# Performance work log

Measured on AMD Instinct MI355X. Metric: run time of the kernel, lower is better.

The kernel has to match this reference:

```python
import jax, jax.numpy as jnp
import numpy as np
import math

B, LQ, LK, D, DV = 16, 2048, 2048, 256, 256


def setup_inputs() -> dict:
    key = jax.random.key(0)
    k1, k2, k3, k4 = jax.random.split(key, 4)
    query = jax.random.normal(k1, (B, LQ, D), dtype=jnp.float32)
    key_t = jax.random.normal(k2, (B, LK, D), dtype=jnp.float32)
    value = jax.random.normal(k3, (B, LK, DV), dtype=jnp.float32)
    valid_length = jax.random.randint(k4, (B,), 0, LK, dtype=jnp.int32)
    return {"query": query, "key": key_t, "value": value, "valid_length": valid_length}


def reference(query, key, value, valid_length):
    # scores: [B, Lq, Lk]
    d = query.shape[-1]
    scores = jnp.einsum("bqd,bkd->bqk", query, key) / math.sqrt(d)
    # SequenceMask in the torch code sets masked positions to 0 (NOT -inf)
    # BEFORE the softmax; reproduce that exact behavior.
    kpos = jnp.arange(scores.shape[-1])  # [Lk]
    mask = kpos[None, None, :] < valid_length[:, None, None]  # [B,1,Lk] -> broadcast over Lq
    scores = jnp.where(mask, scores, 0.0)
    attn = jax.nn.softmax(scores, axis=-1)
    # Dropout is identity in eval mode.
    return jnp.einsum("bqk,bkv->bqv", attn, value)
```

## Files before the change

### kernel.cpp

```cpp
#include <hip/hip_runtime.h>

#define LQg 2048
#define LKg 2048
#define DDg 256
#define NBg 16
#define KVB 32
#define NTILES 64
#define SMAX 2

typedef unsigned int uint;
typedef unsigned short ushort;
typedef unsigned char uchar;
typedef __attribute__((ext_vector_type(8))) __bf16 bf16x8;
typedef __attribute__((ext_vector_type(16))) float f32x16;

static __device__ __forceinline__ uint pack2(float a, float b) {
    ushort ua = __builtin_bit_cast(ushort, (__bf16)a);
    ushort ub = __builtin_bit_cast(ushort, (__bf16)b);
    return (uint)ua | ((uint)ub << 16);
}

static __device__ __forceinline__ f32x16 mfma32(bf16x8 a, bf16x8 b, f32x16 c) {
    return __builtin_amdgcn_mfma_f32_32x32x16_bf16(a, b, c, 0, 0, 0);
}

typedef const __attribute__((address_space(1))) uchar* gas_t;
typedef __attribute__((address_space(3))) uchar* las_t;
static __device__ __forceinline__ void gl_lds16(const void* g, void* l) {
    __builtin_amdgcn_global_load_lds((gas_t)g, (las_t)l, 16, 0, 0);
}

__global__ __launch_bounds__(256) void prep_k(const float* __restrict__ K,
                                              uchar* __restrict__ Kimg) {
    const uint gid = blockIdx.x * 256 + threadIdx.x;
    const uint d8 = gid & 31;
    const uint row = (gid >> 5) & 31;
    const uint t = (gid >> 10) & 63;
    const uint b = gid >> 16;
    const float* src = K + (((size_t)b * LKg + t * KVB + row) * DDg + d8 * 8);
    float4 a = *(const float4*)src;
    float4 c = *(const float4*)(src + 4);
    uint4 u;
    u.x = pack2(a.x, a.y); u.y = pack2(a.z, a.w);
    u.z = pack2(c.x, c.y); u.w = pack2(c.z, c.w);
    const size_t base = ((size_t)(b * NTILES + t)) << 14;
    const uint off = row * 512 + ((d8 * 16) ^ ((row & 7) << 4));
    *(uint4*)(Kimg + base + off) = u;
}

__global__ __launch_bounds__(256) void prep_v(const float* __restrict__ V,
                                              uchar* __restrict__ Vimg) {
    const uint gid = blockIdx.x * 256 + threadIdx.x;
    const uint dv = gid & 255;
    const uint t = (gid >> 8) & 63;
    const uint b = gid >> 14;
    const uint rot = 4 * ((dv >> 1) & 15);
    uchar* base = Vimg + (((size_t)(b * NTILES + t)) << 14) + dv * 64;
    const float* src = V + ((size_t)b * LKg + t * KVB) * DDg + dv;
#pragma unroll
    for (int kq = 0; kq < 8; ++kq) {
        float v0 = src[(kq * 4 + 0) * DDg];
        float v1 = src[(kq * 4 + 1) * DDg];
        float v2 = src[(kq * 4 + 2) * DDg];
        float v3 = src[(kq * 4 + 3) * DDg];
        const uint o = (8 * kq + rot) & 63;
        *(uint*)(base + o) = pack2(v0, v1);
        *(uint*)(base + ((o + 4) & 63)) = pack2(v2, v3);
    }
}

__global__ void tv_partial_k(const float* __restrict__ V, const int* __restrict__ vlen,
                             float* __restrict__ part) {
    const int c = blockIdx.x, b = blockIdx.y, t = threadIdx.x;
    const int vl = vlen[b];
    int bnd = ((vl + 31) >> 5) << 5;
    if (bnd > LKg) bnd = LKg;
    const int k0 = c * 128, k1 = k0 + 128;
    int lo = k0 > bnd ? k0 : bnd;
    float s = 0.f;
    for (int k = lo; k < k1; ++k) s += V[((size_t)(b * LKg + k)) * DDg + t];
    part[(size_t)(b * 16 + c) * DDg + t] = s;
}

__global__ void tv_reduce_k(const float* __restrict__ part, float* __restrict__ TV) {
    const int b = blockIdx.x, t = threadIdx.x;
    float s = 0.f;
    for (int c = 0; c < 16; ++c) s += part[(size_t)(b * 16 + c) * DDg + t];
    TV[b * DDg + t] = s;
}

template <int IMG>
__global__ __launch_bounds__(256, 1) void attn_k(
    const float* __restrict__ Qg, const float* __restrict__ Kg,
    const float* __restrict__ Vg, const uchar* __restrict__ Kimg,
    const uchar* __restrict__ Vimg, const int* __restrict__ vlen,
    const float* __restrict__ TV, float* __restrict__ Og,
    ushort* __restrict__ Pacc, float* __restrict__ Mp, float* __restrict__ Ep,
    int S, int use_tail) {
    __shared__ alignas(16) uchar sK[2][KVB * 512];
    __shared__ alignas(16) uchar sV[2][256 * 64];

    const int tid = threadIdx.x;
    const int lane = tid & 63;
    const int w = tid >> 6;
    const int lq = lane & 31;
    const int h = lane >> 5;
    const int qb = blockIdx.x & 15;
    const int b = blockIdx.x >> 4;
    const int s = blockIdx.y;
    const int q = qb * 128 + w * 32 + lq;
    const int vl = vlen[b];

    const float SCALE = 0.09016844136f;

    const int nt = use_tail ? ((vl + KVB - 1) / KVB) : NTILES;
    const int chunk = (nt + S - 1) / S;
    const int t0 = s * chunk;
    const int t1 = (t0 + chunk < nt) ? (t0 + chunk) : nt;

    if (S > 1 && t0 >= t1) {
        if (h == 0) {
            const size_t pidx = ((size_t)(s * NBg + b)) * LQg + q;
            Mp[pidx] = -1e30f;
            Ep[pidx] = 0.f;
        }
        return;
    }

    const int swzK = (lq & 7) << 4;
    const int rotv = (lq >> 1) * 4;

    int cur = 0;
    if (IMG) {
        const uchar* gK = Kimg + (((size_t)(b * NTILES + t0)) << 14) + tid * 16;
        const uchar* gV = Vimg + (((size_t)(b * NTILES + t0)) << 14) + tid * 16;
#pragma unroll
        for (int i = 0; i < 4; ++i) {
            gl_lds16(gK + i * 4096, &sK[0][i * 4096 + tid * 16]);
            gl_lds16(gV + i * 4096, &sV[0][i * 4096 + tid * 16]);
        }
    }

    bf16x8 qf[16];
    {
        const float* qp = Qg + ((size_t)(b * LQg + q)) * DDg + h * 8;
#pragma unroll
        for (int c = 0; c < 16; ++c) {
            float4 a = *(const float4*)(qp + c * 16);
            float4 bb = *(const float4*)(qp + c * 16 + 4);
            uint4 u;
            u.x = pack2(a.x * SCALE, a.y * SCALE);
            u.y = pack2(a.z * SCALE, a.w * SCALE);
            u.z = pack2(bb.x * SCALE, bb.y * SCALE);
            u.w = pack2(bb.z * SCALE, bb.w * SCALE);
            qf[c] = __builtin_bit_cast(bf16x8, u);
        }
    }

    if (!IMG) {
#pragma unroll
        for (int i = 0; i < 4; ++i) {
            const int cid = i * 256 + tid;
            const int d8 = cid & 31, row = cid >> 5;
            const float* src = Kg + (((size_t)b * LKg + t0 * KVB + row) * DDg + d8 * 8);
            float4 a = *(const float4*)src;
            float4 c = *(const float4*)(src + 4);
            uint4 u;
            u.x = pack2(a.x, a.y); u.y = pack2(a.z, a.w);
            u.z = pack2(c.x, c.y); u.w = pack2(c.z, c.w);
            *(uint4*)(&sK[0][row * 512 + ((d8 * 16) ^ ((row & 7) << 4))]) = u;
        }
        {
            const int dv = tid;
            const uint rot = 4 * ((dv >> 1) & 15);
            const float* src = Vg + ((size_t)b * LKg + t0 * KVB) * DDg + dv;
            uchar* dst = &sV[0][dv * 64];
#pragma unroll
            for (int kq = 0; kq < 8; ++kq) {
                float v0 = src[(kq * 4 + 0) * DDg];
                float v1 = src[(kq * 4 + 1) * DDg];
                float v2 = src[(kq * 4 + 2) * DDg];
                float v3 = src[(kq * 4 + 3) * DDg];
                const uint o = (8 * kq + rot) & 63;
                *(uint*)(dst + o) = pack2(v0, v1);
                *(uint*)(dst + ((o + 4) & 63)) = pack2(v2, v3);
            }
        }
    }

    f32x16 acc[8];
#pragma unroll
    for (int i = 0; i < 8; ++i)
#pragma unroll
        for (int j = 0; j < 16; ++j) acc[i][j] = 0.f;

    float m = -1e30f, ell = 0.f;

    __syncthreads();

    for (int t = t0; t < t1; ++t) {
        const int k0 = t * KVB;

        if (t + 1 < t1) {
            if (IMG) {
                const uchar* gK = Kimg + (((size_t)(b * NTILES + t + 1)) << 14) + tid * 16;
                const uchar* gV = Vimg + (((size_t)(b * NTILES + t + 1)) << 14) + tid * 16;
#pragma unroll
                for (int i = 0; i < 4; ++i) {
                    gl_lds16(gK + i * 4096, &sK[cur ^ 1][i * 4096 + tid * 16]);
                    gl_lds16(gV + i * 4096, &sV[cur ^ 1][i * 4096 + tid * 16]);
                }
            } else {
                const int k1 = (t + 1) * KVB;
#pragma unroll
                for (int i = 0; i < 4; ++i) {
                    const int cid = i * 256 + tid;
                    const int d8 = cid & 31, row = cid >> 5;
                    const float* src = Kg + (((size_t)b * LKg + k1 + row) * DDg + d8 * 8);
                    float4 a = *(const float4*)src;
                    float4 c = *(const float4*)(src + 4);
                    uint4 u;
                    u.x = pack2(a.x, a.y); u.y = pack2(a.z, a.w);
                    u.z = pack2(c.x, c.y); u.w = pack2(c.z, c.w);
                    *(uint4*)(&sK[cur ^ 1][row * 512 + ((d8 * 16) ^ ((row & 7) << 4))]) = u;
                }
                {
                    const int dv = tid;
                    const uint rot = 4 * ((dv >> 1) & 15);
                    const float* src = Vg + ((size_t)b * LKg + k1) * DDg + dv;
                    uchar* dst = &sV[cur ^ 1][dv * 64];
#pragma unroll
                    for (int kq = 0; kq < 8; ++kq) {
                        float v0 = src[(kq * 4 + 0) * DDg];
                        float v1 = src[(kq * 4 + 1) * DDg];
                        float v2 = src[(kq * 4 + 2) * DDg];
                        float v3 = src[(kq * 4 + 3) * DDg];
                        const uint o = (8 * kq + rot) & 63;
                        *(uint*)(dst + o) = pack2(v0, v1);
                        *(uint*)(dst + ((o + 4) & 63)) = pack2(v2, v3);
                    }
                }
            }
        }

        const uchar* sKc = sK[cur];
        const uchar* sVc = sV[cur];
        f32x16 s0;
#pragma unroll
        for (int j = 0; j < 16; ++j) s0[j] = 0.f;
#pragma unroll
        for (int c = 0; c < 16; ++c) {
            bf16x8 kf = *(const bf16x8*)(sKc + lq * 512 + ((c * 32 + h * 16) ^ swzK));
            s0 = mfma32(kf, qf[c], s0);
        }

        if (k0 + KVB > vl) {
            const int kb0 = k0 + 4 * h;
#pragma unroll
            for (int r = 0; r < 16; ++r) {
                const int key0 = kb0 + (r & 3) + 8 * (r >> 2);
                if (key0 >= vl) s0[r] = 0.f;
            }
        }

        float mt = s0[0];
#pragma unroll
        for (int r = 1; r < 16; ++r) mt = fmaxf(mt, s0[r]);
        mt = fmaxf(mt, __shfl_xor(mt, 32));
        if (mt > m + 8.f) {
            const float mn = fmaxf(m, mt);
            const float sf = exp2f(m - mn);
            ell *= sf;
#pragma unroll
            for (int i = 0; i < 8; ++i) acc[i] *= sf;
            m = mn;
        }
        float rs = 0.f;
#pragma unroll
        for (int r = 0; r < 16; ++r) { s0[r] = exp2f(s0[r] - m); rs += s0[r]; }
        rs += __shfl_xor(rs, 32);
        ell += rs;

        bf16x8 pf[2];
#pragma unroll
        for (int kc = 0; kc < 2; ++kc) {
            const int bb = kc * 8;
            uint w0 = pack2(s0[bb + 0], s0[bb + 1]);
            uint w1 = pack2(s0[bb + 2], s0[bb + 3]);
            uint w2 = pack2(s0[bb + 4], s0[bb + 5]);
            uint w3 = pack2(s0[bb + 6], s0[bb + 7]);
            uint e0 = __shfl_xor(w0, 32);
            uint e1 = __shfl_xor(w1, 32);
            uint e2 = __shfl_xor(w2, 32);
            uint e3 = __shfl_xor(w3, 32);
            uint4 u;
            u.x = h ? e2 : w0;
            u.y = h ? e3 : w1;
            u.z = h ? w2 : e0;
            u.w = h ? w3 : e1;
            pf[kc] = __builtin_bit_cast(bf16x8, u);
        }

#pragma unroll
        for (int kc = 0; kc < 2; ++kc) {
            const int kk = kc * 16 + h * 8;
            const uint o0 = (uint)((2 * kk + rotv) & 63);
            const uint o1 = (uint)((2 * kk + 4 + rotv) & 63);
            const uint o2 = (uint)((2 * kk + 8 + rotv) & 63);
            const uint o3 = (uint)((2 * kk + 12 + rotv) & 63);
#pragma unroll
            for (int dt = 0; dt < 8; ++dt) {
                const uchar* base = sVc + dt * 2048 + lq * 64;
                uint4 u;
                u.x = *(const uint*)(base + o0);
                u.y = *(const uint*)(base + o1);
                u.z = *(const uint*)(base + o2);
                u.w = *(const uint*)(base + o3);
                acc[dt] = mfma32(__builtin_bit_cast(bf16x8, u), pf[kc], acc[dt]);
            }
        }

        __syncthreads();
        cur ^= 1;
    }

    if (S > 1) {
        const size_t pidx = ((size_t)(s * NBg + b)) * LQg + q;
        if (h == 0) { Mp[pidx] = m; Ep[pidx] = ell; }
        ushort* pp = Pacc + pidx * DDg;
#pragma unroll
        for (int dt = 0; dt < 8; ++dt) {
#pragma unroll
            for (int rg = 0; rg < 4; ++rg) {
                const int dv0 = dt * 32 + 8 * rg + 4 * h;
                uint2 uu;
                uu.x = pack2(acc[dt][rg * 4 + 0], acc[dt][rg * 4 + 1]);
                uu.y = pack2(acc[dt][rg * 4 + 2], acc[dt][rg * 4 + 3]);
                *(uint2*)(pp + dv0) = uu;
            }
        }
        return;
    }

    if (use_tail) {
        const int bnd = nt * KVB;
        const int cnt = LKg - bnd;
        if (cnt > 0) {
            if (m < -8.f) {
                const float sf = exp2f(m);
                ell *= sf;
#pragma unroll
                for (int i = 0; i < 8; ++i) acc[i] *= sf;
                m = 0.f;
            }
            const float pt = exp2f(-m);
            ell += (float)cnt * pt;
            const float* tp = TV + b * DDg + h * 4;
#pragma unroll
            for (int dt = 0; dt < 8; ++dt) {
#pragma unroll
                for (int rg = 0; rg < 4; ++rg) {
                    float4 tv = *(const float4*)(tp + dt * 32 + rg * 8);
                    acc[dt][rg * 4 + 0] += pt * tv.x;
                    acc[dt][rg * 4 + 1] += pt * tv.y;
                    acc[dt][rg * 4 + 2] += pt * tv.z;
                    acc[dt][rg * 4 + 3] += pt * tv.w;
                }
            }
        }
    }
    const float inv = 1.f / ell;
    float* op = Og + ((size_t)(b * LQg + q)) * DDg + h * 4;
#pragma unroll
    for (int dt = 0; dt < 8; ++dt) {
#pragma unroll
        for (int rg = 0; rg < 4; ++rg) {
            float4 o;
            o.x = acc[dt][rg * 4 + 0] * inv;
            o.y = acc[dt][rg * 4 + 1] * inv;
            o.z = acc[dt][rg * 4 + 2] * inv;
            o.w = acc[dt][rg * 4 + 3] * inv;
            *(float4*)(op + dt * 32 + rg * 8) = o;
        }
    }
}

__global__ void combine_k(const ushort* __restrict__ Pacc, const float* __restrict__ Mp,
                          const float* __restrict__ Ep, const float* __restrict__ TV,
                          const int* __restrict__ vlen, float* __restrict__ Og, int S) {
    const int t = threadIdx.x;
    const int qi = t >> 6;
    const int dv4 = (t & 63) * 4;
    const long long bq0 = (long long)blockIdx.x * 4;
    const int b = (int)(bq0 >> 11);
    const int q = (int)(bq0 & 2047) + qi;
    const int vl = vlen[b];
    int bnd = ((vl + 31) >> 5) << 5;
    if (bnd > LKg) bnd = LKg;
    const int cnt = LKg - bnd;

    float mi[SMAX], ei[SMAX];
    float M = (cnt > 0) ? 0.f : -1e30f;
    for (int s = 0; s < S; ++s) {
        const size_t pidx = ((size_t)(s * NBg + b)) * LQg + q;
        mi[s] = Mp[pidx];
        ei[s] = Ep[pidx];
        if (ei[s] > 0.f) M = fmaxf(M, mi[s]);
    }
    float L = 0.f;
    float o0 = 0.f, o1 = 0.f, o2 = 0.f, o3 = 0.f;
    for (int s = 0; s < S; ++s) {
        if (ei[s] > 0.f) {
            const float wg = exp2f(mi[s] - M);
            L += ei[s] * wg;
            const size_t pidx = ((size_t)(s * NBg + b)) * LQg + q;
            uint2 uu = *(const uint2*)(Pacc + pidx * DDg + dv4);
            o0 += wg * __builtin_bit_cast(float, (uu.x & 0xFFFFu) << 16);
            o1 += wg * __builtin_bit_cast(float, (uu.x & 0xFFFF0000u));
            o2 += wg * __builtin_bit_cast(float, (uu.y & 0xFFFFu) << 16);
            o3 += wg * __builtin_bit_cast(float, (uu.y & 0xFFFF0000u));
        }
    }
    if (cnt > 0) {
        const float pt = exp2f(-M);
        L += (float)cnt * pt;
        float4 tv = *(const float4*)(TV + b * DDg + dv4);
        o0 += pt * tv.x; o1 += pt * tv.y; o2 += pt * tv.z; o3 += pt * tv.w;
    }
    const float inv = 1.f / L;
    float4 o; o.x = o0 * inv; o.y = o1 * inv; o.z = o2 * inv; o.w = o3 * inv;
    *(float4*)(Og + ((size_t)(b * LQg + q)) * DDg + dv4) = o;
}

extern "C" void kernel_launch(void* const* d_in, const int* in_sizes, int n_in,
                              void* d_out, int out_size, void* d_ws, size_t ws_size,
                              hipStream_t stream) {
    const float* Q = (const float*)d_in[0];
    const float* K = (const float*)d_in[1];
    const float* V = (const float*)d_in[2];
    const int* vlen = (const int*)d_in[3];
    float* out = (float*)d_out;

    const size_t off_part = 0;
    const size_t off_TV = 262144;
    const size_t off_K = 524288;
    const size_t imgsz = (size_t)NBg * NTILES * 16384;
    const size_t off_V = off_K + imgsz;
    const size_t off_M = off_V + imgsz;
    const size_t mpsz = (size_t)SMAX * NBg * LQg * 4;
    const size_t off_E = off_M + mpsz;
    const size_t off_P = off_E + mpsz;
    const size_t accsz = (size_t)NBg * LQg * DDg * 2;

    const size_t need_tail = off_TV + (size_t)NBg * DDg * 4;
    const size_t need_img = off_M;
    const size_t need_split = off_P + (size_t)SMAX * accsz;

    const int use_tail = (ws_size >= need_tail) ? 1 : 0;
    const int use_img = (ws_size >= need_img) ? 1 : 0;
    const int S = (use_img && use_tail && ws_size >= need_split) ? SMAX : 1;

    float* part = (float*)((char*)d_ws + off_part);
    float* TV = (float*)((char*)d_ws + off_TV);
    uchar* Kimg = (uchar*)d_ws + off_K;
    uchar* Vimg = (uchar*)d_ws + off_V;
    float* Mp = (float*)((char*)d_ws + off_M);
    float* Ep = (float*)((char*)d_ws + off_E);
    ushort* Pacc = (ushort*)((char*)d_ws + off_P);

    if (use_tail) {
        tv_partial_k<<<dim3(16, 16), 256, 0, stream>>>(V, vlen, part);
        tv_reduce_k<<<dim3(16), 256, 0, stream>>>(part, TV);
    }
    if (use_img) {
        prep_k<<<dim3(4096), 256, 0, stream>>>(K, Kimg);
        prep_v<<<dim3(1024), 256, 0, stream>>>(V, Vimg);
        attn_k<1><<<dim3(256, S), 256, 0, stream>>>(Q, K, V, Kimg, Vimg, vlen, TV, out,
                                                    Pacc, Mp, Ep, S, use_tail);
    } else {
        attn_k<0><<<dim3(256, 1), 256, 0, stream>>>(Q, K, V, Kimg, Vimg, vlen, TV, out,
                                                    Pacc, Mp, Ep, 1, use_tail);
    }
    if (S > 1) {
        combine_k<<<dim3(NBg * LQg / 4), 256, 0, stream>>>(Pacc, Mp, Ep, TV, vlen, out, S);
    }
}
```

Before: 217.1 us.

## Double KV tile to 64 keys, add phase-rotated tile order and MFMA priority

Result: faster. 207.7 us (-4.4%).

```diff
diff --git a/kernel.cpp b/kernel.cpp
--- a/kernel.cpp
+++ b/kernel.cpp
@@ -4,8 +4,9 @@
 #define LKg 2048
 #define DDg 256
 #define NBg 16
-#define KVB 32
-#define NTILES 64
+#define KVB 64
+#define NTILES 32
+#define TSHIFT 15
 #define SMAX 2
 
 typedef unsigned int uint;
@@ -24,6 +25,10 @@
     return __builtin_amdgcn_mfma_f32_32x32x16_bf16(a, b, c, 0, 0, 0);
 }
 
+static __device__ __forceinline__ int vrot(int dv) {
+    return (((dv & 15) * 8) + (((dv >> 2) & 7) * 16)) & 127;
+}
+
 typedef const __attribute__((address_space(1))) uchar* gas_t;
 typedef __attribute__((address_space(3))) uchar* las_t;
 static __device__ __forceinline__ void gl_lds16(const void* g, void* l) {
@@ -34,8 +39,8 @@
                                               uchar* __restrict__ Kimg) {
     const uint gid = blockIdx.x * 256 + threadIdx.x;
     const uint d8 = gid & 31;
-    const uint row = (gid >> 5) & 31;
-    const uint t = (gid >> 10) & 63;
+    const uint row = (gid >> 5) & 63;
+    const uint t = (gid >> 11) & 31;
     const uint b = gid >> 16;
     const float* src = K + (((size_t)b * LKg + t * KVB + row) * DDg + d8 * 8);
     float4 a = *(const float4*)src;
@@ -43,7 +48,7 @@
     uint4 u;
     u.x = pack2(a.x, a.y); u.y = pack2(a.z, a.w);
     u.z = pack2(c.x, c.y); u.w = pack2(c.z, c.w);
-    const size_t base = ((size_t)(b * NTILES + t)) << 14;
+    const size_t base = ((size_t)(b * NTILES + t)) << TSHIFT;
     const uint off = row * 512 + ((d8 * 16) ^ ((row & 7) << 4));
     *(uint4*)(Kimg + base + off) = u;
 }
@@ -52,20 +57,20 @@
                                               uchar* __restrict__ Vimg) {
     const uint gid = blockIdx.x * 256 + threadIdx.x;
     const uint dv = gid & 255;
-    const uint t = (gid >> 8) & 63;
-    const uint b = gid >> 14;
-    const uint rot = 4 * ((dv >> 1) & 15);
-    uchar* base = Vimg + (((size_t)(b * NTILES + t)) << 14) + dv * 64;
+    const uint t = (gid >> 8) & 31;
+    const uint b = gid >> 13;
+    const uint rot = (uint)vrot((int)dv);
+    uchar* base = Vimg + (((size_t)(b * NTILES + t)) << TSHIFT) + dv * 128;
     const float* src = V + ((size_t)b * LKg + t * KVB) * DDg + dv;
 #pragma unroll
-    for (int kq = 0; kq < 8; ++kq) {
+    for (int kq = 0; kq < 16; ++kq) {
         float v0 = src[(kq * 4 + 0) * DDg];
         float v1 = src[(kq * 4 + 1) * DDg];
         float v2 = src[(kq * 4 + 2) * DDg];
         float v3 = src[(kq * 4 + 3) * DDg];
-        const uint o = (8 * kq + rot) & 63;
-        *(uint*)(base + o) = pack2(v0, v1);
-        *(uint*)(base + ((o + 4) & 63)) = pack2(v2, v3);
+        const uint o = (8 * kq + rot) & 127;
+        uint2 uu; uu.x = pack2(v0, v1); uu.y = pack2(v2, v3);
+        *(uint2*)(base + o) = uu;
     }
 }
 
@@ -73,7 +78,7 @@
                              float* __restrict__ part) {
     const int c = blockIdx.x, b = blockIdx.y, t = threadIdx.x;
     const int vl = vlen[b];
-    int bnd = ((vl + 31) >> 5) << 5;
+    int bnd = ((vl + 63) >> 6) << 6;
     if (bnd > LKg) bnd = LKg;
     const int k0 = c * 128, k1 = k0 + 128;
     int lo = k0 > bnd ? k0 : bnd;
@@ -98,7 +103,7 @@
     ushort* __restrict__ Pacc, float* __restrict__ Mp, float* __restrict__ Ep,
     int S, int use_tail) {
     __shared__ alignas(16) uchar sK[2][KVB * 512];
-    __shared__ alignas(16) uchar sV[2][256 * 64];
+    __shared__ alignas(16) uchar sV[2][256 * 128];
 
     const int tid = threadIdx.x;
     const int lane = tid & 63;
@@ -128,14 +133,18 @@
     }
 
     const int swzK = (lq & 7) << 4;
-    const int rotv = (lq >> 1) * 4;
+    const int rotv = vrot(lq);
+
+    const int len = t1 - t0;
+    const int ph = ((blockIdx.x ^ s) & 1) ? (len >> 1) : 0;
+    const int ts0 = t0 + ph;
 
     int cur = 0;
     if (IMG) {
-        const uchar* gK = Kimg + (((size_t)(b * NTILES + t0)) << 14) + tid * 16;
-        const uchar* gV = Vimg + (((size_t)(b * NTILES + t0)) << 14) + tid * 16;
-#pragma unroll
-        for (int i = 0; i < 4; ++i) {
+        const uchar* gK = Kimg + (((size_t)(b * NTILES + ts0)) << TSHIFT) + tid * 16;
+        const uchar* gV = Vimg + (((size_t)(b * NTILES + ts0)) << TSHIFT) + tid * 16;
+#pragma unroll
+        for (int i = 0; i < 8; ++i) {
             gl_lds16(gK + i * 4096, &sK[0][i * 4096 + tid * 16]);
             gl_lds16(gV + i * 4096, &sV[0][i * 4096 + tid * 16]);
         }
@@ -159,10 +168,10 @@
 
     if (!IMG) {
 #pragma unroll
-        for (int i = 0; i < 4; ++i) {
+        for (int i = 0; i < 8; ++i) {
             const int cid = i * 256 + tid;
             const int d8 = cid & 31, row = cid >> 5;
-            const float* src = Kg + (((size_t)b * LKg + t0 * KVB + row) * DDg + d8 * 8);
+            const float* src = Kg + (((size_t)b * LKg + ts0 * KVB + row) * DDg + d8 * 8);
             float4 a = *(const float4*)src;
             float4 c = *(const float4*)(src + 4);
             uint4 u;
@@ -172,18 +181,18 @@
         }
         {
             const int dv = tid;
-            const uint rot = 4 * ((dv >> 1) & 15);
-            const float* src = Vg + ((size_t)b * LKg + t0 * KVB) * DDg + dv;
-            uchar* dst = &sV[0][dv * 64];
-#pragma unroll
-            for (int kq = 0; kq < 8; ++kq) {
+            const uint rot = (uint)vrot(dv);
+            const float* src = Vg + ((size_t)b * LKg + ts0 * KVB) * DDg + dv;
+            uchar* dst = &sV[0][dv * 128];
+#pragma unroll
+            for (int kq = 0; kq < 16; ++kq) {
                 float v0 = src[(kq * 4 + 0) * DDg];
                 float v1 = src[(kq * 4 + 1) * DDg];
                 float v2 = src[(kq * 4 + 2) * DDg];
                 float v3 = src[(kq * 4 + 3) * DDg];
-                const uint o = (8 * kq + rot) & 63;
-                *(uint*)(dst + o) = pack2(v0, v1);
-                *(uint*)(dst + ((o + 4) & 63)) = pack2(v2, v3);
+                const uint o = (8 * kq + rot) & 127;
+                uint2 uu; uu.x = pack2(v0, v1); uu.y = pack2(v2, v3);
+                *(uint2*)(dst + o) = uu;
             }
         }
     }
@@ -198,23 +207,25 @@
 
     __syncthreads();
 
-    for (int t = t0; t < t1; ++t) {
-        const int k0 = t * KVB;
-
-        if (t + 1 < t1) {
+    int tt = ts0;
+    for (int i = 0; i < len; ++i) {
+        const int tn = (tt + 1 == t1) ? t0 : tt + 1;
+        const int k0 = tt * KVB;
+
+        if (i + 1 < len) {
             if (IMG) {
-                const uchar* gK = Kimg + (((size_t)(b * NTILES + t + 1)) << 14) + tid * 16;
-                const uchar* gV = Vimg + (((size_t)(b * NTILES + t + 1)) << 14) + tid * 16;
-#pragma unroll
-                for (int i = 0; i < 4; ++i) {
-                    gl_lds16(gK + i * 4096, &sK[cur ^ 1][i * 4096 + tid * 16]);
-                    gl_lds16(gV + i * 4096, &sV[cur ^ 1][i * 4096 + tid * 16]);
+                const uchar* gK = Kimg + (((size_t)(b * NTILES + tn)) << TSHIFT) + tid * 16;
+                const uchar* gV = Vimg + (((size_t)(b * NTILES + tn)) << TSHIFT) + tid * 16;
+#pragma unroll
+                for (int j = 0; j < 8; ++j) {
+                    gl_lds16(gK + j * 4096, &sK[cur ^ 1][j * 4096 + tid * 16]);
+                    gl_lds16(gV + j * 4096, &sV[cur ^ 1][j * 4096 + tid * 16]);
                 }
             } else {
-                const int k1 = (t + 1) * KVB;
-#pragma unroll
-                for (int i = 0; i < 4; ++i) {
-                    const int cid = i * 256 + tid;
+                const int k1 = tn * KVB;
+#pragma unroll
+                for (int j = 0; j < 8; ++j) {
+                    const int cid = j * 256 + tid;
                     const int d8 = cid & 31, row = cid >> 5;
                     const float* src = Kg + (((size_t)b * LKg + k1 + row) * DDg + d8 * 8);
                     float4 a = *(const float4*)src;
@@ -226,18 +237,18 @@
                 }
                 {
                     const int dv = tid;
-                    const uint rot = 4 * ((dv >> 1) & 15);
+                    const uint rot = (uint)vrot(dv);
                     const float* src = Vg + ((size_t)b * LKg + k1) * DDg + dv;
-                    uchar* dst = &sV[cur ^ 1][dv * 64];
-#pragma unroll
-                    for (int kq = 0; kq < 8; ++kq) {
+                    uchar* dst = &sV[cur ^ 1][dv * 128];
+#pragma unroll
+                    for (int kq = 0; kq < 16; ++kq) {
                         float v0 = src[(kq * 4 + 0) * DDg];
                         float v1 = src[(kq * 4 + 1) * DDg];
                         float v2 = src[(kq * 4 + 2) * DDg];
                         float v3 = src[(kq * 4 + 3) * DDg];
-                        const uint o = (8 * kq + rot) & 63;
-                        *(uint*)(dst + o) = pack2(v0, v1);
-                        *(uint*)(dst + ((o + 4) & 63)) = pack2(v2, v3);
+                        const uint o = (8 * kq + rot) & 127;
+                        uint2 uu; uu.x = pack2(v0, v1); uu.y = pack2(v2, v3);
+                        *(uint2*)(dst + o) = uu;
                     }
                 }
             }
@@ -245,14 +256,19 @@
 
         const uchar* sKc = sK[cur];
         const uchar* sVc = sV[cur];
-        f32x16 s0;
-#pragma unroll
-        for (int j = 0; j < 16; ++j) s0[j] = 0.f;
+        f32x16 s0, s1;
+#pragma unroll
+        for (int j = 0; j < 16; ++j) { s0[j] = 0.f; s1[j] = 0.f; }
+        __builtin_amdgcn_s_setprio(1);
 #pragma unroll
         for (int c = 0; c < 16; ++c) {
-            bf16x8 kf = *(const bf16x8*)(sKc + lq * 512 + ((c * 32 + h * 16) ^ swzK));
-            s0 = mfma32(kf, qf[c], s0);
-        }
+            const int inner = (c * 32 + h * 16) ^ swzK;
+            bf16x8 kf0 = *(const bf16x8*)(sKc + lq * 512 + inner);
+            bf16x8 kf1 = *(const bf16x8*)(sKc + (32 + lq) * 512 + inner);
+            s0 = mfma32(kf0, qf[c], s0);
+            s1 = mfma32(kf1, qf[c], s1);
+        }
+        __builtin_amdgcn_s_setprio(0);
 
         if (k0 + KVB > vl) {
             const int kb0 = k0 + 4 * h;
@@ -260,35 +276,41 @@
             for (int r = 0; r < 16; ++r) {
                 const int key0 = kb0 + (r & 3) + 8 * (r >> 2);
                 if (key0 >= vl) s0[r] = 0.f;
+                if (key0 + 32 >= vl) s1[r] = 0.f;
             }
         }
 
         float mt = s0[0];
 #pragma unroll
         for (int r = 1; r < 16; ++r) mt = fmaxf(mt, s0[r]);
+#pragma unroll
+        for (int r = 0; r < 16; ++r) mt = fmaxf(mt, s1[r]);
         mt = fmaxf(mt, __shfl_xor(mt, 32));
         if (mt > m + 8.f) {
             const float mn = fmaxf(m, mt);
             const float sf = exp2f(m - mn);
             ell *= sf;
 #pragma unroll
-            for (int i = 0; i < 8; ++i) acc[i] *= sf;
+            for (int i2 = 0; i2 < 8; ++i2) acc[i2] *= sf;
             m = mn;
         }
         float rs = 0.f;
 #pragma unroll
         for (int r = 0; r < 16; ++r) { s0[r] = exp2f(s0[r] - m); rs += s0[r]; }
+#pragma unroll
+        for (int r = 0; r < 16; ++r) { s1[r] = exp2f(s1[r] - m); rs += s1[r]; }
         rs += __shfl_xor(rs, 32);
         ell += rs;
 
-        bf16x8 pf[2];
-#pragma unroll
-        for (int kc = 0; kc < 2; ++kc) {
-            const int bb = kc * 8;
-            uint w0 = pack2(s0[bb + 0], s0[bb + 1]);
-            uint w1 = pack2(s0[bb + 2], s0[bb + 3]);
-            uint w2 = pack2(s0[bb + 4], s0[bb + 5]);
-            uint w3 = pack2(s0[bb + 6], s0[bb + 7]);
+        bf16x8 pf[4];
+#pragma unroll
+        for (int kc = 0; kc < 4; ++kc) {
+            const f32x16& ps = (kc < 2) ? s0 : s1;
+            const int bb = (kc & 1) * 8;
+            uint w0 = pack2(ps[bb + 0], ps[bb + 1]);
+            uint w1 = pack2(ps[bb + 2], ps[bb + 3]);
+            uint w2 = pack2(ps[bb + 4], ps[bb + 5]);
+            uint w3 = pack2(ps[bb + 6], ps[bb + 7]);
             uint e0 = __shfl_xor(w0, 32);
             uint e1 = __shfl_xor(w1, 32);
             uint e2 = __shfl_xor(w2, 32);
@@ -301,27 +323,26 @@
             pf[kc] = __builtin_bit_cast(bf16x8, u);
         }
 
-#pragma unroll
-        for (int kc = 0; kc < 2; ++kc) {
+        __builtin_amdgcn_s_setprio(1);
+#pragma unroll
+        for (int kc = 0; kc < 4; ++kc) {
             const int kk = kc * 16 + h * 8;
-            const uint o0 = (uint)((2 * kk + rotv) & 63);
-            const uint o1 = (uint)((2 * kk + 4 + rotv) & 63);
-            const uint o2 = (uint)((2 * kk + 8 + rotv) & 63);
-            const uint o3 = (uint)((2 * kk + 12 + rotv) & 63);
+            const uint o0 = (uint)((2 * kk + rotv) & 127);
+            const uint o1 = (uint)((2 * (kk + 4) + rotv) & 127);
 #pragma unroll
             for (int dt = 0; dt < 8; ++dt) {
-                const uchar* base = sVc + dt * 2048 + lq * 64;
-                uint4 u;
-                u.x = *(const uint*)(base + o0);
-                u.y = *(const uint*)(base + o1);
-                u.z = *(const uint*)(base + o2);
-                u.w = *(const uint*)(base + o3);
+                const uchar* base = sVc + dt * 4096 + lq * 128;
+                uint2 a = *(const uint2*)(base + o0);
+                uint2 c2 = *(const uint2*)(base + o1);
+                uint4 u; u.x = a.x; u.y = a.y; u.z = c2.x; u.w = c2.y;
                 acc[dt] = mfma32(__builtin_bit_cast(bf16x8, u), pf[kc], acc[dt]);
             }
         }
+        __builtin_amdgcn_s_setprio(0);
 
         __syncthreads();
         cur ^= 1;
+        tt = tn;
     }
 
     if (S > 1) {
@@ -395,7 +416,7 @@
     const int b = (int)(bq0 >> 11);
     const int q = (int)(bq0 & 2047) + qi;
     const int vl = vlen[b];
-    int bnd = ((vl + 31) >> 5) << 5;
+    int bnd = ((vl + 63) >> 6) << 6;
     if (bnd > LKg) bnd = LKg;
     const int cnt = LKg - bnd;
 
@@ -444,7 +465,7 @@
     const size_t off_part = 0;
     const size_t off_TV = 262144;
     const size_t off_K = 524288;
-    const size_t imgsz = (size_t)NBg * NTILES * 16384;
+    const size_t imgsz = (size_t)NBg * NTILES << TSHIFT;
     const size_t off_V = off_K + imgsz;
     const size_t off_M = off_V + imgsz;
     const size_t mpsz = (size_t)SMAX * NBg * LQg * 4;
@@ -474,7 +495,7 @@
     }
     if (use_img) {
         prep_k<<<dim3(4096), 256, 0, stream>>>(K, Kimg);
-        prep_v<<<dim3(1024), 256, 0, stream>>>(V, Vimg);
+        prep_v<<<dim3(512), 256, 0, stream>>>(V, Vimg);
         attn_k<1><<<dim3(256, S), 256, 0, stream>>>(Q, K, V, Kimg, Vimg, vlen, TV, out,
                                                     Pacc, Mp, Ep, S, use_tail);
     } else {
```
